# Kernel tuning notes

Measured on AMD Instinct MI355X. Metric: run time of the kernel, lower is better.

Reference implementation:

```python
import jax, jax.numpy as jnp
import numpy as np


def setup_inputs() -> dict:
    key = jax.random.key(0)
    ks = jax.random.split(key, 16)
    B, T, H = 64, 512, 256
    s = lambda n: 1.0 / np.sqrt(n)
    return {
        "q_vec": jax.random.normal(ks[0], (B, H), jnp.float32),
        "fact_vecs": jax.random.normal(ks[1], (B, T, H), jnp.float32),
        "input_len": jax.random.randint(ks[2], (B,), 1, T + 1, jnp.int32),
        "W1": jax.random.normal(ks[3], (7 * H, H), jnp.float32) * s(7 * H),
        "b1": jnp.zeros((H,), jnp.float32),
        "W2": jax.random.normal(ks[4], (H, 1), jnp.float32) * s(H),
        "b2": jnp.zeros((1,), jnp.float32),
        "Wr": jax.random.normal(ks[5], (H, H), jnp.float32) * s(H),
        "Ur": jax.random.normal(ks[6], (H, H), jnp.float32) * s(H),
        "br": jnp.zeros((H,), jnp.float32),
        "Wh": jax.random.normal(ks[7], (H, H), jnp.float32) * s(H),
        "Uh": jax.random.normal(ks[8], (H, H), jnp.float32) * s(H),
        "bh": jnp.zeros((H,), jnp.float32),
        "Ws": jax.random.normal(ks[9], (2 * H, 1), jnp.float32) * s(2 * H),
        "bs": jnp.zeros((1,), jnp.float32),
        "We": jax.random.normal(ks[10], (2 * H, 1), jnp.float32) * s(2 * H),
        "be": jnp.zeros((1,), jnp.float32),
    }


def reference(q_vec, fact_vecs, input_len, W1, b1, W2, b2,
              Wr, Ur, br, Wh, Uh, bh, Ws, bs, We, be):
    B, T, H = fact_vecs.shape
    m = q_vec  # prev_memory = q_vec (never actually updated in the original inference loop)
    qb = jnp.broadcast_to(q_vec[:, None, :], (B, T, H))
    mb = qb  # m == q_vec
    f = fact_vecs
    # episodic attention features: [f, m, q, f*q, f*m, |f-q|, |f-m|] -> [B,T,7H]
    feats = jnp.concatenate(
        [f, mb, qb, f * qb, f * mb, jnp.abs(f - qb), jnp.abs(f - mb)], axis=-1)
    att = jnp.tanh(feats @ W1 + b1) @ W2 + b2          # [B,T,1]
    g = jax.nn.softmax(att[..., 0], axis=1)            # [B,T]

    # AttentionGRU scan over time with sequence-length masking (dynamic_rnn semantics)
    valid = (jnp.arange(T)[:, None] < input_len[None, :])  # [T,B]

    def step(h, inp):
        x_t, g_t, v_t = inp  # [B,H], [B], [B]
        r = jax.nn.sigmoid(x_t @ Wr + h @ Ur + br)
        hc = jnp.tanh(x_t @ Wh + (r * h) @ Uh + bh)
        hn = g_t[:, None] * hc + (1.0 - g_t[:, None]) * h
        hn = jnp.where(v_t[:, None], hn, h)
        out = jnp.where(v_t[:, None], hn, jnp.zeros_like(hn))
        return hn, out

    xs = (jnp.swapaxes(fact_vecs, 0, 1), g.T, valid)
    _, outs = jax.lax.scan(step, jnp.zeros((B, H), fact_vecs.dtype), xs)
    e_outputs = jnp.swapaxes(outs, 0, 1)               # [B,T,H]

    # predict_position (final hop, is_iteration=False): tanh dense over [prev_memory, e_t]
    cat = jnp.concatenate([jnp.broadcast_to(m[:, None, :], (B, T, H)), e_outputs], axis=-1)
    out_s = jnp.tanh(cat @ Ws + bs)[..., 0]            # [B,T]
    out_e = jnp.tanh(cat @ We + be)[..., 0]            # [B,T]
    return out_s, out_e
```

## Files before the change

kernel.cpp:

```cpp
#include <hip/hip_runtime.h>
#include <cstddef>


static __device__ __forceinline__ float b2f(unsigned short u) {
  return __uint_as_float(((unsigned)u) << 16);
}
static __device__ __forceinline__ float blo(unsigned w) { return __uint_as_float(w << 16); }
static __device__ __forceinline__ float bhi(unsigned w) { return __uint_as_float(w & 0xffff0000u); }
static __device__ __forceinline__ unsigned short f2b(float f) {
  unsigned u = __float_as_uint(f);
  u += 0x7fffu + ((u >> 16) & 1u);
  return (unsigned short)(u >> 16);
}
static __device__ __forceinline__ float ldf(const void* b, size_t i, int md) {
  return md ? ((const float*)b)[i] : b2f(((const unsigned short*)b)[i]);
}
static __device__ __forceinline__ unsigned short ldb(const void* b, size_t i, int md) {
  return md ? f2b(((const float*)b)[i]) : ((const unsigned short*)b)[i];
}

typedef short bfrag __attribute__((ext_vector_type(8)));
typedef float f32x4 __attribute__((ext_vector_type(4)));

template <int CTRL>
static __device__ __forceinline__ float dpp_add(float x) {
  int v = __builtin_amdgcn_update_dpp(0, __float_as_int(x), CTRL, 0xF, 0xF, true);
  return x + __int_as_float(v);
}
static __device__ __forceinline__ float red16(float x) {
  x = dpp_add<0xB1>(x);
  x = dpp_add<0x4E>(x);
  x = dpp_add<0x141>(x);
  x = dpp_add<0x140>(x);
  return x;
}
static __device__ __forceinline__ void sync_lds() {
  __builtin_amdgcn_fence(__ATOMIC_RELEASE, "workgroup", "local");
  __builtin_amdgcn_s_barrier();
  __builtin_amdgcn_fence(__ATOMIC_ACQUIRE, "workgroup", "local");
}
static __device__ __forceinline__ float fast_tanh(float x) {
  float xc = fminf(fmaxf(x, -15.f), 15.f);
  return 1.f - 2.f * __builtin_amdgcn_rcpf(__expf(2.f * xc) + 1.f);
}

__global__ void k_detect(const void* __restrict__ fact, int* __restrict__ mode) {
  int tid = threadIdx.x;
  const unsigned short* u = (const unsigned short*)fact;
  float v = fabsf(b2f(u[2 * tid]));
  if (!(v == v)) v = 1e30f;
  for (int o = 32; o > 0; o >>= 1) v = fmaxf(v, __shfl_xor(v, o));
  __shared__ float red[4];
  int wave = tid >> 6, lane = tid & 63;
  if (lane == 0) red[wave] = v;
  __syncthreads();
  if (tid == 0) {
    float m = fmaxf(fmaxf(red[0], red[1]), fmaxf(red[2], red[3]));
    mode[0] = (m > 1e4f) ? 1 : 0;
  }
}

__global__ void k_prep_w(const void* __restrict__ W1,
                         const void* __restrict__ Wr,
                         const void* __restrict__ Wh,
                         const void* __restrict__ Ur,
                         const void* __restrict__ Uh,
                         const int* __restrict__ mode,
                         unsigned* __restrict__ W5q,
                         unsigned* __restrict__ Urp,
                         unsigned* __restrict__ Uhp) {
  int md = *mode;
  int idx = blockIdx.x * 256 + threadIdx.x;
  int i = idx >> 8, j = idx & 255;
  Urp[idx] = (unsigned)ldb(Ur, (size_t)(2 * i) * 256 + j, md) |
             ((unsigned)ldb(Ur, (size_t)(2 * i + 1) * 256 + j, md) << 16);
  Uhp[idx] = (unsigned)ldb(Uh, (size_t)(2 * i) * 256 + j, md) |
             ((unsigned)ldb(Uh, (size_t)(2 * i + 1) * 256 + j, md) << 16);
  float v0, v1;
  int p;
  p = i;
  v0 = ldf(W1, (size_t)(2 * i) * 256 + j, md);
  v1 = ldf(W1, (size_t)(2 * i + 1) * 256 + j, md);
  W5q[(((p >> 2) * 256 + j) << 2) + (p & 3)] = (unsigned)f2b(v0) | ((unsigned)f2b(v1) << 16);
  p = 128 + i;
  v0 = ldf(W1, (size_t)(768 + 2 * i) * 256 + j, md) + ldf(W1, (size_t)(1024 + 2 * i) * 256 + j, md);
  v1 = ldf(W1, (size_t)(769 + 2 * i) * 256 + j, md) + ldf(W1, (size_t)(1025 + 2 * i) * 256 + j, md);
  W5q[(((p >> 2) * 256 + j) << 2) + (p & 3)] = (unsigned)f2b(v0) | ((unsigned)f2b(v1) << 16);
  p = 256 + i;
  v0 = ldf(W1, (size_t)(1280 + 2 * i) * 256 + j, md) + ldf(W1, (size_t)(1536 + 2 * i) * 256 + j, md);
  v1 = ldf(W1, (size_t)(1281 + 2 * i) * 256 + j, md) + ldf(W1, (size_t)(1537 + 2 * i) * 256 + j, md);
  W5q[(((p >> 2) * 256 + j) << 2) + (p & 3)] = (unsigned)f2b(v0) | ((unsigned)f2b(v1) << 16);
  p = 384 + i;
  v0 = ldf(Wr, (size_t)(2 * i) * 256 + j, md);
  v1 = ldf(Wr, (size_t)(2 * i + 1) * 256 + j, md);
  W5q[(((p >> 2) * 256 + j) << 2) + (p & 3)] = (unsigned)f2b(v0) | ((unsigned)f2b(v1) << 16);
  p = 512 + i;
  v0 = ldf(Wh, (size_t)(2 * i) * 256 + j, md);
  v1 = ldf(Wh, (size_t)(2 * i + 1) * 256 + j, md);
  W5q[(((p >> 2) * 256 + j) << 2) + (p & 3)] = (unsigned)f2b(v0) | ((unsigned)f2b(v1) << 16);
}

__global__ void k_prep_q(const void* __restrict__ q,
                         const void* __restrict__ W1,
                         const void* __restrict__ b1,
                         const void* __restrict__ Ws,
                         const void* __restrict__ bs,
                         const void* __restrict__ We,
                         const void* __restrict__ be,
                         const int* __restrict__ mode,
                         float* __restrict__ qw1,
                         float* __restrict__ qs,
                         float* __restrict__ qe) {
  __shared__ float qsh[256];
  __shared__ float reds[4], rede[4];
  int md = *mode;
  int b = blockIdx.x, tid = threadIdx.x;
  float qv = ldf(q, (size_t)b * 256 + tid, md);
  qsh[tid] = qv;
  __syncthreads();
  float acc = ldf(b1, tid, md);
  for (int i = 0; i < 256; ++i) {
    float w = ldf(W1, (size_t)(256 + i) * 256 + tid, md) + ldf(W1, (size_t)(512 + i) * 256 + tid, md);
    acc = fmaf(qsh[i], w, acc);
  }
  qw1[b * 256 + tid] = acc;
  float ps = qv * ldf(Ws, tid, md);
  float pe = qv * ldf(We, tid, md);
  for (int o = 32; o > 0; o >>= 1) { ps += __shfl_down(ps, o); pe += __shfl_down(pe, o); }
  int wave = tid >> 6, lane = tid & 63;
  if (lane == 0) { reds[wave] = ps; rede[wave] = pe; }
  __syncthreads();
  if (tid == 0) {
    qs[b] = ldf(bs, 0, md) + reds[0] + reds[1] + reds[2] + reds[3];
    qe[b] = ldf(be, 0, md) + rede[0] + rede[1] + rede[2] + rede[3];
  }
}

__launch_bounds__(256, 2)
__global__ void k_main(const void* __restrict__ fact,
                       const void* __restrict__ q,
                       const unsigned* __restrict__ W5q,
                       const float* __restrict__ qw1,
                       const void* __restrict__ W2,
                       const void* __restrict__ b2v,
                       const void* __restrict__ br,
                       const void* __restrict__ bh,
                       const int* __restrict__ mode,
                       float* __restrict__ att,
                       unsigned* __restrict__ xrh) {
  __shared__ __align__(16) unsigned short A[32 * 776];
  __shared__ float wsc[128];
  int md = *mode;
  int blk = blockIdx.x;
  int b = blk >> 4, t0 = (blk & 15) * 32;
  int tid = threadIdx.x;
  {
    float qv = ldf(q, (size_t)b * 256 + tid, md);
    for (int r = 0; r < 32; ++r) {
      float f = ldf(fact, ((size_t)(b * 512 + t0 + r)) * 256 + tid, md);
      A[r * 776 + tid] = f2b(f);
      A[r * 776 + 256 + tid] = f2b(f * qv);
      A[r * 776 + 512 + tid] = f2b(fabsf(f - qv));
    }
  }
  __syncthreads();
  int wv = tid >> 6, lane = tid & 63;
  int n16 = lane & 15, quad = lane >> 4;
  int colb = wv * 64 + n16;
  const uint4* W4 = (const uint4*)W5q;
  f32x4 z = {0.f, 0.f, 0.f, 0.f};
  f32x4 u[2][4], ar[2][4], ah[2][4];
#pragma unroll
  for (int rt = 0; rt < 2; ++rt)
#pragma unroll
    for (int tile = 0; tile < 4; ++tile) { u[rt][tile] = z; ar[rt][tile] = z; ah[rt][tile] = z; }
#pragma unroll
  for (int kc = 0; kc < 8; ++kc) {
    uint4 av0 = *(const uint4*)((const char*)A + n16 * 1552 + kc * 64 + quad * 16);
    uint4 av1 = *(const uint4*)((const char*)A + (16 + n16) * 1552 + kc * 64 + quad * 16);
    bfrag af0 = __builtin_bit_cast(bfrag, av0);
    bfrag af1 = __builtin_bit_cast(bfrag, av1);
    int pg = kc * 4 + quad;
#pragma unroll
    for (int tile = 0; tile < 4; ++tile) {
      int col = colb + tile * 16;
      uint4 bu = W4[(size_t)pg * 256 + col];
      uint4 bw = W4[(size_t)(96 + pg) * 256 + col];
      uint4 bv = W4[(size_t)(128 + pg) * 256 + col];
      bfrag bfu = __builtin_bit_cast(bfrag, bu);
      bfrag bfw = __builtin_bit_cast(bfrag, bw);
      bfrag bfv = __builtin_bit_cast(bfrag, bv);
      u[0][tile] = __builtin_amdgcn_mfma_f32_16x16x32_bf16(af0, bfu, u[0][tile], 0, 0, 0);
      u[1][tile] = __builtin_amdgcn_mfma_f32_16x16x32_bf16(af1, bfu, u[1][tile], 0, 0, 0);
      ar[0][tile] = __builtin_amdgcn_mfma_f32_16x16x32_bf16(af0, bfw, ar[0][tile], 0, 0, 0);
      ar[1][tile] = __builtin_amdgcn_mfma_f32_16x16x32_bf16(af1, bfw, ar[1][tile], 0, 0, 0);
      ah[0][tile] = __builtin_amdgcn_mfma_f32_16x16x32_bf16(af0, bfv, ah[0][tile], 0, 0, 0);
      ah[1][tile] = __builtin_amdgcn_mfma_f32_16x16x32_bf16(af1, bfv, ah[1][tile], 0, 0, 0);
    }
  }
#pragma unroll
  for (int kc = 8; kc < 24; ++kc) {
    uint4 av0 = *(const uint4*)((const char*)A + n16 * 1552 + kc * 64 + quad * 16);
    uint4 av1 = *(const uint4*)((const char*)A + (16 + n16) * 1552 + kc * 64 + quad * 16);
    bfrag af0 = __builtin_bit_cast(bfrag, av0);
    bfrag af1 = __builtin_bit_cast(bfrag, av1);
    int pg = kc * 4 + quad;
#pragma unroll
    for (int tile = 0; tile < 4; ++tile) {
      int col = colb + tile * 16;
      uint4 bu = W4[(size_t)pg * 256 + col];
      bfrag bfu = __builtin_bit_cast(bfrag, bu);
      u[0][tile] = __builtin_amdgcn_mfma_f32_16x16x32_bf16(af0, bfu, u[0][tile], 0, 0, 0);
      u[1][tile] = __builtin_amdgcn_mfma_f32_16x16x32_bf16(af1, bfu, u[1][tile], 0, 0, 0);
    }
  }
  float qwv[4], w2v[4], brv[4], bhv[4];
#pragma unroll
  for (int tile = 0; tile < 4; ++tile) {
    int col = colb + tile * 16;
    qwv[tile] = qw1[b * 256 + col];
    w2v[tile] = ldf(W2, col, md);
    brv[tile] = ldf(br, col, md);
    bhv[tile] = ldf(bh, col, md);
  }
  float ps[2][4];
#pragma unroll
  for (int rt = 0; rt < 2; ++rt)
#pragma unroll
    for (int reg = 0; reg < 4; ++reg) {
      float p = 0.f;
#pragma unroll
      for (int tile = 0; tile < 4; ++tile) {
        float hid = fast_tanh(u[rt][tile][reg] + qwv[tile]);
        p = fmaf(hid, w2v[tile], p);
      }
      ps[rt][reg] = red16(p);
    }
  if (n16 == 0) {
#pragma unroll
    for (int rt = 0; rt < 2; ++rt)
#pragma unroll
      for (int reg = 0; reg < 4; ++reg) wsc[rt * 64 + wv * 16 + quad * 4 + reg] = ps[rt][reg];
  }
  __syncthreads();
  if (tid < 32) {
    int rt = tid >> 4, tl = tid & 15;
    att[b * 512 + t0 + rt * 16 + tl] =
        wsc[rt * 64 + tl] + wsc[rt * 64 + 16 + tl] + wsc[rt * 64 + 32 + tl] + wsc[rt * 64 + 48 + tl] +
        ldf(b2v, 0, md);
  }
#pragma unroll
  for (int rt = 0; rt < 2; ++rt)
#pragma unroll
    for (int tile = 0; tile < 4; ++tile) {
      int col = colb + tile * 16;
#pragma unroll
      for (int reg = 0; reg < 4; ++reg) {
        int t = t0 + rt * 16 + quad * 4 + reg;
        unsigned v = (unsigned)f2b(ar[rt][tile][reg] + brv[tile]) |
                     ((unsigned)f2b(ah[rt][tile][reg] + bhv[tile]) << 16);
        xrh[((size_t)(b * 512 + t)) * 256 + col] = v;
      }
    }
}

__global__ void k_softmax(const float* __restrict__ att, float* __restrict__ g) {
  __shared__ float red[8];
  int b = blockIdx.x, tid = threadIdx.x;
  float v = att[b * 512 + tid];
  float m = v;
  for (int o = 32; o > 0; o >>= 1) m = fmaxf(m, __shfl_xor(m, o));
  int wave = tid >> 6, lane = tid & 63;
  if (lane == 0) red[wave] = m;
  __syncthreads();
  m = red[0];
#pragma unroll
  for (int w = 1; w < 8; ++w) m = fmaxf(m, red[w]);
  float e = __expf(v - m);
  float s = e;
  for (int o = 32; o > 0; o >>= 1) s += __shfl_xor(s, o);
  __syncthreads();
  if (lane == 0) red[wave] = s;
  __syncthreads();
  s = red[0] + red[1] + red[2] + red[3] + red[4] + red[5] + red[6] + red[7];
  g[b * 512 + tid] = e / s;
}

__launch_bounds__(512, 2)
__global__ void k_scan(const unsigned* __restrict__ Urp,
                       const unsigned* __restrict__ Uhp,
                       const unsigned* __restrict__ xrh,
                       const float* __restrict__ g,
                       const int* __restrict__ input_len,
                       const void* __restrict__ Ws,
                       const void* __restrict__ We,
                       const float* __restrict__ qs,
                       const float* __restrict__ qe,
                       const int* __restrict__ mode,
                       float* __restrict__ out) {
  __shared__ __align__(16) unsigned short hB[4 * 272];
  __shared__ __align__(16) unsigned short rhB[4 * 272];
  __shared__ float sacc[4][512];
  __shared__ float eacc[4][512];
  int md = *mode;
  int b0 = blockIdx.x * 4;
  int tid = threadIdx.x;
  int wv = tid >> 6, lane = tid & 63;
  int n16 = lane & 15, quad = lane >> 4;
  int col0 = wv * 32 + n16;
  int col1 = col0 + 16;
  uint4 br4[2][8], bh4[2][8];
#pragma unroll
  for (int tile = 0; tile < 2; ++tile) {
    int col = wv * 32 + tile * 16 + n16;
#pragma unroll
    for (int kc = 0; kc < 8; ++kc) {
      int p = kc * 16 + quad * 4;
      uint4 rv = {Urp[(size_t)p * 256 + col], Urp[(size_t)(p + 1) * 256 + col],
                  Urp[(size_t)(p + 2) * 256 + col], Urp[(size_t)(p + 3) * 256 + col]};
      uint4 hv = {Uhp[(size_t)p * 256 + col], Uhp[(size_t)(p + 1) * 256 + col],
                  Uhp[(size_t)(p + 2) * 256 + col], Uhp[(size_t)(p + 3) * 256 + col]};
      br4[tile][kc] = rv;
      bh4[tile][kc] = hv;
    }
  }
  for (int i = tid; i < 4 * 272; i += 512) { hB[i] = 0; rhB[i] = 0; }
  for (int i = tid; i < 2048; i += 512) { ((float*)sacc)[i] = 0.f; ((float*)eacc)[i] = 0.f; }
  int mylen = input_len[b0 + quad];
  float ws0 = ldf(Ws, 256 + col0, md), ws1 = ldf(Ws, 256 + col1, md);
  float we0 = ldf(We, 256 + col0, md), we1 = ldf(We, 256 + col1, md);
  float hm0 = 0.f, hm1 = 0.f;
  float pend_s = 0.f, pend_e = 0.f;
  int pend_T = 0;
  const char* hbase = (const char*)hB + (n16 >> 2) * 544 + quad * 16;
  const char* rhbase = (const char*)rhB + (n16 >> 2) * 544 + quad * 16;
  const unsigned* xrow = xrh + (size_t)(b0 + quad) * 512 * 256;
  const float* grow = g + (size_t)(b0 + quad) * 512;

  unsigned xa[16], xbb[16];
  float4 ga0, ga1, gb0, gb1;
  auto prefetch = [&](int tb, unsigned (&xr)[16], float4& g0, float4& g1) {
    const unsigned* xp = xrow + (size_t)tb * 8 * 256;
#pragma unroll
    for (int s = 0; s < 8; ++s) {
      xr[2 * s] = xp[s * 256 + col0];
      xr[2 * s + 1] = xp[s * 256 + col1];
    }
    const float* gp = grow + tb * 8;
    g0 = *(const float4*)gp;
    g1 = *(const float4*)(gp + 4);
  };
  prefetch(0, xa, ga0, ga1);
  __syncthreads();
  const f32x4 z4 = {0.f, 0.f, 0.f, 0.f};

  auto step = [&](int T, unsigned XC0, unsigned XC1, float GT) {
    f32x4 accA[2][4];
#pragma unroll
    for (int tl = 0; tl < 2; ++tl)
#pragma unroll
      for (int j = 0; j < 4; ++j) accA[tl][j] = z4;
#pragma unroll
    for (int kc = 0; kc < 8; ++kc) {
      uint4 av = *(const uint4*)(hbase + kc * 64);
      bfrag af = __builtin_bit_cast(bfrag, av);
      int j = kc & 3;
      accA[0][j] = __builtin_amdgcn_mfma_f32_16x16x32_bf16(af, __builtin_bit_cast(bfrag, br4[0][kc]), accA[0][j], 0, 0, 0);
      accA[1][j] = __builtin_amdgcn_mfma_f32_16x16x32_bf16(af, __builtin_bit_cast(bfrag, br4[1][kc]), accA[1][j], 0, 0, 0);
    }
    {
      float rs = red16(pend_s);
      float re_ = red16(pend_e);
      if (n16 == 0) {
        atomicAdd(&sacc[quad][pend_T], rs);
        atomicAdd(&eacc[quad][pend_T], re_);
      }
    }
    {
      float v0 = (accA[0][0][0] + accA[0][1][0]) + (accA[0][2][0] + accA[0][3][0]);
      float v1 = (accA[1][0][0] + accA[1][1][0]) + (accA[1][2][0] + accA[1][3][0]);
      float e0 = __expf(-(v0 + blo(XC0)));
      float e1 = __expf(-(v1 + blo(XC1)));
      float r0 = __builtin_amdgcn_rcpf(1.f + e0);
      float r1 = __builtin_amdgcn_rcpf(1.f + e1);
      rhB[quad * 272 + col0] = f2b(r0 * hm0);
      rhB[quad * 272 + col1] = f2b(r1 * hm1);
    }
    sync_lds();
    f32x4 accB[2][4];
#pragma unroll
    for (int tl = 0; tl < 2; ++tl)
#pragma unroll
      for (int j = 0; j < 4; ++j) accB[tl][j] = z4;
#pragma unroll
    for (int kc = 0; kc < 8; ++kc) {
      uint4 av = *(const uint4*)(rhbase + kc * 64);
      bfrag af = __builtin_bit_cast(bfrag, av);
      int j = kc & 3;
      accB[0][j] = __builtin_amdgcn_mfma_f32_16x16x32_bf16(af, __builtin_bit_cast(bfrag, bh4[0][kc]), accB[0][j], 0, 0, 0);
      accB[1][j] = __builtin_amdgcn_mfma_f32_16x16x32_bf16(af, __builtin_bit_cast(bfrag, bh4[1][kc]), accB[1][j], 0, 0, 0);
    }
    {
      float w0 = (accB[0][0][0] + accB[0][1][0]) + (accB[0][2][0] + accB[0][3][0]);
      float w1 = (accB[1][0][0] + accB[1][1][0]) + (accB[1][2][0] + accB[1][3][0]);
      float c0 = fminf(fmaxf(w0 + bhi(XC0), -15.f), 15.f);
      float c1 = fminf(fmaxf(w1 + bhi(XC1), -15.f), 15.f);
      float hc0 = 1.f - 2.f * __builtin_amdgcn_rcpf(__expf(2.f * c0) + 1.f);
      float hc1 = 1.f - 2.f * __builtin_amdgcn_rcpf(__expf(2.f * c1) + 1.f);
      bool valid = T < mylen;
      float hn0 = hm0 + GT * (hc0 - hm0);
      float hn1 = hm1 + GT * (hc1 - hm1);
      hm0 = valid ? hn0 : hm0;
      hm1 = valid ? hn1 : hm1;
      hB[quad * 272 + col0] = f2b(hm0);
      hB[quad * 272 + col1] = f2b(hm1);
      pend_s = valid ? fmaf(hm0, ws0, hm1 * ws1) : 0.f;
      pend_e = valid ? fmaf(hm0, we0, hm1 * we1) : 0.f;
      pend_T = T;
    }
    sync_lds();
  };

  for (int tb2 = 0; tb2 < 32; ++tb2) {
    prefetch(2 * tb2 + 1, xbb, gb0, gb1);
#pragma unroll
    for (int tt = 0; tt < 8; ++tt)
      step(tb2 * 16 + tt, xa[2 * tt], xa[2 * tt + 1], tt < 4 ? ga0[tt] : ga1[tt - 4]);
    prefetch(tb2 < 31 ? 2 * tb2 + 2 : 63, xa, ga0, ga1);
#pragma unroll
    for (int tt = 0; tt < 8; ++tt)
      step(tb2 * 16 + 8 + tt, xbb[2 * tt], xbb[2 * tt + 1], tt < 4 ? gb0[tt] : gb1[tt - 4]);
  }
  {
    float rs = red16(pend_s);
    float re_ = red16(pend_e);
    if (n16 == 0) {
      atomicAdd(&sacc[quad][pend_T], rs);
      atomicAdd(&eacc[quad][pend_T], re_);
    }
  }
  sync_lds();
  for (int i = tid; i < 2048; i += 512) {
    int b = i >> 9, t = i & 511;
    int row = (b0 + b) * 512 + t;
    out[row] = tanhf(qs[b0 + b] + sacc[b][t]);
    out[32768 + row] = tanhf(qe[b0 + b] + eacc[b][t]);
  }
}

extern "C" void kernel_launch(void* const* d_in, const int* in_sizes, int n_in,
                              void* d_out, int out_size, void* d_ws, size_t ws_size,
                              hipStream_t stream) {
  const void* q    = d_in[0];
  const void* fact = d_in[1];
  const int* ilen  = (const int*)d_in[2];
  const void* W1   = d_in[3];
  const void* b1   = d_in[4];
  const void* W2   = d_in[5];
  const void* b2v  = d_in[6];
  const void* Wr   = d_in[7];
  const void* Ur   = d_in[8];
  const void* br   = d_in[9];
  const void* Wh   = d_in[10];
  const void* Uh   = d_in[11];
  const void* bh   = d_in[12];
  const void* Ws   = d_in[13];
  const void* bs   = d_in[14];
  const void* We   = d_in[15];
  const void* be   = d_in[16];

  char* w = (char*)d_ws;
  unsigned* W5q = (unsigned*)(w);
  unsigned* Urp = (unsigned*)(w + 1310720);
  unsigned* Uhp = (unsigned*)(w + 1441792);
  float*    qw1 = (float*)(w + 1572864);
  float*    qs  = (float*)(w + 1638400);
  float*    qe  = (float*)(w + 1638656);
  float*    att = (float*)(w + 1638912);
  float*    g   = (float*)(w + 1769984);
  unsigned* xrh = (unsigned*)(w + 1901056);
  int*      mode = (int*)(w + 52232704);
  float* out = (float*)d_out;

  k_detect<<<dim3(1), dim3(256), 0, stream>>>(fact, mode);
  k_prep_w<<<dim3(128), dim3(256), 0, stream>>>(W1, Wr, Wh, Ur, Uh, mode, W5q, Urp, Uhp);
  k_prep_q<<<dim3(64), dim3(256), 0, stream>>>(q, W1, b1, Ws, bs, We, be, mode, qw1, qs, qe);
  k_main<<<dim3(1024), dim3(256), 0, stream>>>(fact, q, W5q, qw1, W2, b2v, br, bh, mode, att, xrh);
  k_softmax<<<dim3(64), dim3(512), 0, stream>>>(att, g);
  k_scan<<<dim3(16), dim3(512), 0, stream>>>(Urp, Uhp, xrh, g, ilen, Ws, We, qs, qe, mode, out);
}
```

Before: 659.1 us.

## Inline dtype detection, fuse softmax into scan, vectorize feature tile loads

Removes the separate detect kernel by having each kernel compute the input mode with a wave-level reduction. The softmax kernel is removed and its work is done inside the scan kernel, which keeps gate values in shared memory instead of global memory. The feature-tile build in the main kernel now uses 4-wide loads and packed stores. This cuts two kernel launches and a global round trip, at the cost of repeated detection work and extra barriers at the start of the scan.

```diff
diff --git a/kernel.cpp b/kernel.cpp
--- a/kernel.cpp
+++ b/kernel.cpp
@@ -18,6 +18,30 @@
 static __device__ __forceinline__ unsigned short ldb(const void* b, size_t i, int md) {
   return md ? f2b(((const float*)b)[i]) : ((const unsigned short*)b)[i];
 }
+static __device__ __forceinline__ unsigned pack2(float a, float b) {
+  return (unsigned)f2b(a) | ((unsigned)f2b(b) << 16);
+}
+static __device__ __forceinline__ int detect_mode(const void* fact) {
+  const unsigned short* u = (const unsigned short*)fact;
+  int lane = threadIdx.x & 63;
+  float v = 0.f;
+#pragma unroll
+  for (int k = 0; k < 4; ++k) {
+    float x = fabsf(b2f(u[2 * (lane + 64 * k)]));
+    x = (x == x) ? x : 1e30f;
+    v = fmaxf(v, x);
+  }
+  for (int o = 32; o > 0; o >>= 1) v = fmaxf(v, __shfl_xor(v, o));
+  return v > 1e4f ? 1 : 0;
+}
+static __device__ __forceinline__ float4 ld4(const void* p, size_t i, int md) {
+  if (md) return *(const float4*)((const float*)p + i);
+  const unsigned short* u = (const unsigned short*)p + i;
+  uint2 w = *(const uint2*)u;
+  float4 r;
+  r.x = blo(w.x); r.y = bhi(w.x); r.z = blo(w.y); r.w = bhi(w.y);
+  return r;
+}
 
 typedef short bfrag __attribute__((ext_vector_type(8)));
 typedef float f32x4 __attribute__((ext_vector_type(4)));
@@ -44,32 +68,16 @@
   return 1.f - 2.f * __builtin_amdgcn_rcpf(__expf(2.f * xc) + 1.f);
 }
 
-__global__ void k_detect(const void* __restrict__ fact, int* __restrict__ mode) {
-  int tid = threadIdx.x;
-  const unsigned short* u = (const unsigned short*)fact;
-  float v = fabsf(b2f(u[2 * tid]));
-  if (!(v == v)) v = 1e30f;
-  for (int o = 32; o > 0; o >>= 1) v = fmaxf(v, __shfl_xor(v, o));
-  __shared__ float red[4];
-  int wave = tid >> 6, lane = tid & 63;
-  if (lane == 0) red[wave] = v;
-  __syncthreads();
-  if (tid == 0) {
-    float m = fmaxf(fmaxf(red[0], red[1]), fmaxf(red[2], red[3]));
-    mode[0] = (m > 1e4f) ? 1 : 0;
-  }
-}
-
-__global__ void k_prep_w(const void* __restrict__ W1,
+__global__ void k_prep_w(const void* __restrict__ fact,
+                         const void* __restrict__ W1,
                          const void* __restrict__ Wr,
                          const void* __restrict__ Wh,
                          const void* __restrict__ Ur,
                          const void* __restrict__ Uh,
-                         const int* __restrict__ mode,
                          unsigned* __restrict__ W5q,
                          unsigned* __restrict__ Urp,
                          unsigned* __restrict__ Uhp) {
-  int md = *mode;
+  int md = detect_mode(fact);
   int idx = blockIdx.x * 256 + threadIdx.x;
   int i = idx >> 8, j = idx & 255;
   Urp[idx] = (unsigned)ldb(Ur, (size_t)(2 * i) * 256 + j, md) |
@@ -81,39 +89,39 @@
   p = i;
   v0 = ldf(W1, (size_t)(2 * i) * 256 + j, md);
   v1 = ldf(W1, (size_t)(2 * i + 1) * 256 + j, md);
-  W5q[(((p >> 2) * 256 + j) << 2) + (p & 3)] = (unsigned)f2b(v0) | ((unsigned)f2b(v1) << 16);
+  W5q[(((p >> 2) * 256 + j) << 2) + (p & 3)] = pack2(v0, v1);
   p = 128 + i;
   v0 = ldf(W1, (size_t)(768 + 2 * i) * 256 + j, md) + ldf(W1, (size_t)(1024 + 2 * i) * 256 + j, md);
   v1 = ldf(W1, (size_t)(769 + 2 * i) * 256 + j, md) + ldf(W1, (size_t)(1025 + 2 * i) * 256 + j, md);
-  W5q[(((p >> 2) * 256 + j) << 2) + (p & 3)] = (unsigned)f2b(v0) | ((unsigned)f2b(v1) << 16);
+  W5q[(((p >> 2) * 256 + j) << 2) + (p & 3)] = pack2(v0, v1);
   p = 256 + i;
   v0 = ldf(W1, (size_t)(1280 + 2 * i) * 256 + j, md) + ldf(W1, (size_t)(1536 + 2 * i) * 256 + j, md);
   v1 = ldf(W1, (size_t)(1281 + 2 * i) * 256 + j, md) + ldf(W1, (size_t)(1537 + 2 * i) * 256 + j, md);
-  W5q[(((p >> 2) * 256 + j) << 2) + (p & 3)] = (unsigned)f2b(v0) | ((unsigned)f2b(v1) << 16);
+  W5q[(((p >> 2) * 256 + j) << 2) + (p & 3)] = pack2(v0, v1);
   p = 384 + i;
   v0 = ldf(Wr, (size_t)(2 * i) * 256 + j, md);
   v1 = ldf(Wr, (size_t)(2 * i + 1) * 256 + j, md);
-  W5q[(((p >> 2) * 256 + j) << 2) + (p & 3)] = (unsigned)f2b(v0) | ((unsigned)f2b(v1) << 16);
+  W5q[(((p >> 2) * 256 + j) << 2) + (p & 3)] = pack2(v0, v1);
   p = 512 + i;
   v0 = ldf(Wh, (size_t)(2 * i) * 256 + j, md);
   v1 = ldf(Wh, (size_t)(2 * i + 1) * 256 + j, md);
-  W5q[(((p >> 2) * 256 + j) << 2) + (p & 3)] = (unsigned)f2b(v0) | ((unsigned)f2b(v1) << 16);
-}
-
-__global__ void k_prep_q(const void* __restrict__ q,
+  W5q[(((p >> 2) * 256 + j) << 2) + (p & 3)] = pack2(v0, v1);
+}
+
+__global__ void k_prep_q(const void* __restrict__ fact,
+                         const void* __restrict__ q,
                          const void* __restrict__ W1,
                          const void* __restrict__ b1,
                          const void* __restrict__ Ws,
                          const void* __restrict__ bs,
                          const void* __restrict__ We,
                          const void* __restrict__ be,
-                         const int* __restrict__ mode,
                          float* __restrict__ qw1,
                          float* __restrict__ qs,
                          float* __restrict__ qe) {
   __shared__ float qsh[256];
   __shared__ float reds[4], rede[4];
-  int md = *mode;
+  int md = detect_mode(fact);
   int b = blockIdx.x, tid = threadIdx.x;
   float qv = ldf(q, (size_t)b * 256 + tid, md);
   qsh[tid] = qv;
@@ -145,22 +153,30 @@
                        const void* __restrict__ b2v,
                        const void* __restrict__ br,
                        const void* __restrict__ bh,
-                       const int* __restrict__ mode,
                        float* __restrict__ att,
                        unsigned* __restrict__ xrh) {
   __shared__ __align__(16) unsigned short A[32 * 776];
   __shared__ float wsc[128];
-  int md = *mode;
+  int md = detect_mode(fact);
   int blk = blockIdx.x;
   int b = blk >> 4, t0 = (blk & 15) * 32;
   int tid = threadIdx.x;
   {
-    float qv = ldf(q, (size_t)b * 256 + tid, md);
-    for (int r = 0; r < 32; ++r) {
-      float f = ldf(fact, ((size_t)(b * 512 + t0 + r)) * 256 + tid, md);
-      A[r * 776 + tid] = f2b(f);
-      A[r * 776 + 256 + tid] = f2b(f * qv);
-      A[r * 776 + 512 + tid] = f2b(fabsf(f - qv));
+    int c4 = (tid & 63) * 4;
+    int rg = tid >> 6;
+    float4 q4 = ld4(q, (size_t)b * 256 + c4, md);
+#pragma unroll
+    for (int s = 0; s < 8; ++s) {
+      int r = rg * 8 + s;
+      float4 f4 = ld4(fact, ((size_t)(b * 512 + t0 + r)) * 256 + c4, md);
+      char* base = (char*)A + (size_t)r * 1552 + (size_t)c4 * 2;
+      uint2 w0 = {pack2(f4.x, f4.y), pack2(f4.z, f4.w)};
+      uint2 w1 = {pack2(f4.x * q4.x, f4.y * q4.y), pack2(f4.z * q4.z, f4.w * q4.w)};
+      uint2 w2 = {pack2(fabsf(f4.x - q4.x), fabsf(f4.y - q4.y)),
+                  pack2(fabsf(f4.z - q4.z), fabsf(f4.w - q4.w))};
+      *(uint2*)(base) = w0;
+      *(uint2*)(base + 512) = w1;
+      *(uint2*)(base + 1024) = w2;
     }
   }
   __syncthreads();
@@ -264,45 +280,25 @@
     }
 }
 
-__global__ void k_softmax(const float* __restrict__ att, float* __restrict__ g) {
-  __shared__ float red[8];
-  int b = blockIdx.x, tid = threadIdx.x;
-  float v = att[b * 512 + tid];
-  float m = v;
-  for (int o = 32; o > 0; o >>= 1) m = fmaxf(m, __shfl_xor(m, o));
-  int wave = tid >> 6, lane = tid & 63;
-  if (lane == 0) red[wave] = m;
-  __syncthreads();
-  m = red[0];
-#pragma unroll
-  for (int w = 1; w < 8; ++w) m = fmaxf(m, red[w]);
-  float e = __expf(v - m);
-  float s = e;
-  for (int o = 32; o > 0; o >>= 1) s += __shfl_xor(s, o);
-  __syncthreads();
-  if (lane == 0) red[wave] = s;
-  __syncthreads();
-  s = red[0] + red[1] + red[2] + red[3] + red[4] + red[5] + red[6] + red[7];
-  g[b * 512 + tid] = e / s;
-}
-
 __launch_bounds__(512, 2)
 __global__ void k_scan(const unsigned* __restrict__ Urp,
                        const unsigned* __restrict__ Uhp,
                        const unsigned* __restrict__ xrh,
-                       const float* __restrict__ g,
+                       const float* __restrict__ att,
                        const int* __restrict__ input_len,
                        const void* __restrict__ Ws,
                        const void* __restrict__ We,
                        const float* __restrict__ qs,
                        const float* __restrict__ qe,
-                       const int* __restrict__ mode,
+                       const void* __restrict__ fact,
                        float* __restrict__ out) {
   __shared__ __align__(16) unsigned short hB[4 * 272];
   __shared__ __align__(16) unsigned short rhB[4 * 272];
   __shared__ float sacc[4][512];
   __shared__ float eacc[4][512];
-  int md = *mode;
+  __shared__ float gbuf[4][512];
+  __shared__ float redx[8];
+  int md = detect_mode(fact);
   int b0 = blockIdx.x * 4;
   int tid = threadIdx.x;
   int wv = tid >> 6, lane = tid & 63;
@@ -326,6 +322,25 @@
   }
   for (int i = tid; i < 4 * 272; i += 512) { hB[i] = 0; rhB[i] = 0; }
   for (int i = tid; i < 2048; i += 512) { ((float*)sacc)[i] = 0.f; ((float*)eacc)[i] = 0.f; }
+#pragma unroll
+  for (int bb = 0; bb < 4; ++bb) {
+    float v = att[(size_t)(b0 + bb) * 512 + tid];
+    float m = v;
+    for (int o = 32; o > 0; o >>= 1) m = fmaxf(m, __shfl_xor(m, o));
+    if (lane == 0) redx[wv] = m;
+    __syncthreads();
+    m = redx[0];
+#pragma unroll
+    for (int w = 1; w < 8; ++w) m = fmaxf(m, redx[w]);
+    float e = __expf(v - m);
+    float s = e;
+    for (int o = 32; o > 0; o >>= 1) s += __shfl_xor(s, o);
+    __syncthreads();
+    if (lane == 0) redx[wv] = s;
+    __syncthreads();
+    s = redx[0] + redx[1] + redx[2] + redx[3] + redx[4] + redx[5] + redx[6] + redx[7];
+    gbuf[bb][tid] = e / s;
+  }
   int mylen = input_len[b0 + quad];
   float ws0 = ldf(Ws, 256 + col0, md), ws1 = ldf(Ws, 256 + col1, md);
   float we0 = ldf(We, 256 + col0, md), we1 = ldf(We, 256 + col1, md);
@@ -335,10 +350,10 @@
   const char* hbase = (const char*)hB + (n16 >> 2) * 544 + quad * 16;
   const char* rhbase = (const char*)rhB + (n16 >> 2) * 544 + quad * 16;
   const unsigned* xrow = xrh + (size_t)(b0 + quad) * 512 * 256;
-  const float* grow = g + (size_t)(b0 + quad) * 512;
 
   unsigned xa[16], xbb[16];
   float4 ga0, ga1, gb0, gb1;
+  __syncthreads();
   auto prefetch = [&](int tb, unsigned (&xr)[16], float4& g0, float4& g1) {
     const unsigned* xp = xrow + (size_t)tb * 8 * 256;
 #pragma unroll
@@ -346,12 +361,10 @@
       xr[2 * s] = xp[s * 256 + col0];
       xr[2 * s + 1] = xp[s * 256 + col1];
     }
-    const float* gp = grow + tb * 8;
-    g0 = *(const float4*)gp;
-    g1 = *(const float4*)(gp + 4);
+    g0 = *(const float4*)&gbuf[quad][tb * 8];
+    g1 = *(const float4*)&gbuf[quad][tb * 8 + 4];
   };
   prefetch(0, xa, ga0, ga1);
-  __syncthreads();
   const f32x4 z4 = {0.f, 0.f, 0.f, 0.f};
 
   auto step = [&](int T, unsigned XC0, unsigned XC1, float GT) {
@@ -477,15 +490,11 @@
   float*    qs  = (float*)(w + 1638400);
   float*    qe  = (float*)(w + 1638656);
   float*    att = (float*)(w + 1638912);
-  float*    g   = (float*)(w + 1769984);
   unsigned* xrh = (unsigned*)(w + 1901056);
-  int*      mode = (int*)(w + 52232704);
   float* out = (float*)d_out;
 
-  k_detect<<<dim3(1), dim3(256), 0, stream>>>(fact, mode);
-  k_prep_w<<<dim3(128), dim3(256), 0, stream>>>(W1, Wr, Wh, Ur, Uh, mode, W5q, Urp, Uhp);
-  k_prep_q<<<dim3(64), dim3(256), 0, stream>>>(q, W1, b1, Ws, bs, We, be, mode, qw1, qs, qe);
-  k_main<<<dim3(1024), dim3(256), 0, stream>>>(fact, q, W5q, qw1, W2, b2v, br, bh, mode, att, xrh);
-  k_softmax<<<dim3(64), dim3(512), 0, stream>>>(att, g);
-  k_scan<<<dim3(16), dim3(512), 0, stream>>>(Urp, Uhp, xrh, g, ilen, Ws, We, qs, qe, mode, out);
-}
+  k_prep_w<<<dim3(128), dim3(256), 0, stream>>>(fact, W1, Wr, Wh, Ur, Uh, W5q, Urp, Uhp);
+  k_prep_q<<<dim3(64), dim3(256), 0, stream>>>(fact, q, W1, b1, Ws, bs, We, be, qw1, qs, qe);
+  k_main<<<dim3(1024), dim3(256), 0, stream>>>(fact, q, W5q, qw1, W2, b2v, br, bh, att, xrh);
+  k_scan<<<dim3(16), dim3(512), 0, stream>>>(Urp, Uhp, xrh, att, ilen, Ws, We, qs, qe, fact, out);
+}
```

After: 655.5 us. No clear change (-0.5%).
